# Kernel tuning notes

Measured on AMD Instinct MI355X. Metric: run time of the kernel, lower is better.

## Reference

```python
import jax, jax.numpy as jnp
import numpy as np

B_, L, DM = 4, 1024, 1024
DI, DS, DR, DC = 1024, 16, 64, 4
NH = 4
DK = DM // NH


def setup_inputs() -> dict:
    key = jax.random.key(0)
    ks = jax.random.split(key, 16)
    def w(i, shape, scale=0.02):
        return jax.random.normal(ks[i], shape, dtype=jnp.float32) * scale
    inp = {
        "x": jax.random.normal(ks[0], (B_, L, DM), dtype=jnp.float32),
        "xx": jax.random.normal(ks[1], (B_, L, DI), dtype=jnp.float32),
        "in_proj_w": w(2, (DI, DM)),
        "conv_w": w(3, (DI, 1, DC)),            # depthwise conv, groups=DI
        "conv_b": jnp.zeros((DI,), jnp.float32),
        "x_proj_w": w(4, (DR + 2 * DS, DI)),
        "dt_proj_w": w(5, (DI, DR)),
        "dt_proj_b": jnp.zeros((DI,), jnp.float32),
        "A_log": jnp.log(jnp.tile(jnp.arange(1, DS + 1, dtype=jnp.float32)[None, :], (DI, 1))),
        "D": jnp.ones((DI,), jnp.float32),
        "wq": w(6, (DM, DM)), "bq": jnp.zeros((DM,), jnp.float32),
        "wk": w(7, (DM, DM)), "bk": jnp.zeros((DM,), jnp.float32),
        "wv": w(8, (DM, DM)), "bv": jnp.zeros((DM,), jnp.float32),
        "wo": w(9, (DM, DM)), "bo": jnp.zeros((DM,), jnp.float32),
    }
    return inp


def _stim_forward(x, xx, in_proj_w, conv_w, conv_b, x_proj_w, dt_proj_w, dt_proj_b,
                  A_log, D, wq, bq, wk, bk, wv, bv, wo, bo):
    b, l, _ = xx.shape
    # query branch: in_proj (Linear, no bias)
    q = x @ in_proj_w.T                                    # (b, l, DI)
    # kv branch: causal depthwise conv1d (padding d_conv-1, truncated to l)
    xc = jnp.transpose(xx, (0, 2, 1))                      # (b, DI, l)
    xc = jax.lax.conv_general_dilated(
        xc, conv_w, window_strides=(1,), padding=[(DC - 1, 0)],
        dimension_numbers=("NCH", "OIH", "NCH"), feature_group_count=DI)
    xc = xc + conv_b[None, :, None]
    u = jax.nn.silu(jnp.transpose(xc, (0, 2, 1)))          # (b, l, DI)
    # SSM parameter projections
    A = -jnp.exp(A_log)                                    # (DI, DS)
    x_dbl = u @ x_proj_w.T                                 # (b, l, DR+2*DS)
    delta, Bm, Cm = jnp.split(x_dbl, [DR, DR + DS], axis=-1)
    delta = jax.nn.softplus(delta @ dt_proj_w.T + dt_proj_b)  # (b, l, DI)
    deltaA = jnp.exp(jnp.einsum("bld,dn->bldn", delta, A))    # (b, l, DI, DS)
    deltaBu = jnp.einsum("bld,bln,bld->bldn", delta, Bm, u)   # (b, l, DI, DS)
    # selective scan over time
    def step(h, inp):
        dA_t, dBu_t, C_t = inp
        h = dA_t * h + dBu_t                               # (b, DI, DS)
        y_t = jnp.einsum("bdn,bn->bd", h, C_t)             # (b, DI)
        return h, y_t
    h0 = jnp.zeros((b, DI, DS), dtype=u.dtype)
    _, ys = jax.lax.scan(step, h0, (jnp.moveaxis(deltaA, 1, 0),
                                    jnp.moveaxis(deltaBu, 1, 0),
                                    jnp.moveaxis(Cm, 1, 0)))
    y = jnp.moveaxis(ys, 0, 1) + u * D                     # (b, l, DI)
    # cross attention: query = q, key/value = y
    Q = (q @ wq.T + bq).reshape(b, l, NH, DK).transpose(0, 2, 1, 3)
    K = (y @ wk.T + bk).reshape(b, l, NH, DK).transpose(0, 2, 1, 3)
    V = (y @ wv.T + bv).reshape(b, l, NH, DK).transpose(0, 2, 1, 3)
    scale = 1.0 / np.sqrt(DK).astype(np.float32)
    scores = jnp.einsum("bhqd,bhkd->bhqk", Q, K) * scale
    attn = jax.nn.softmax(scores, axis=-1)
    out = jnp.einsum("bhqk,bhkd->bhqd", attn, V)
    out = out.transpose(0, 2, 1, 3).reshape(b, l, DM)
    return out @ wo.T + bo


def reference(x, xx, in_proj_w, conv_w, conv_b, x_proj_w, dt_proj_w, dt_proj_b,
              A_log, D, wq, bq, wk, bk, wv, bv, wo, bo):
    return _stim_forward(x, xx, in_proj_w, conv_w, conv_b, x_proj_w, dt_proj_w,
                         dt_proj_b, A_log, D, wq, bq, wk, bk, wv, bv, wo, bo)
```

## Files before the change

### kernel.cpp

```cpp
#include <hip/hip_runtime.h>
#include <math.h>

#define B_  4
#define L_  1024
#define DM  1024
#define DI  1024
#define DS  16
#define DR  64
#define DCV 4
#define NH  4
#define DK  256

#define NCH 32
#define CHL (L_ / NCH)

typedef __attribute__((ext_vector_type(8))) short short8;
typedef __attribute__((ext_vector_type(4))) float floatx4;

static __device__ __forceinline__ unsigned short f2bf(float f) {
    unsigned int u = __float_as_uint(f);
    u += 0x7fffu + ((u >> 16) & 1u);
    return (unsigned short)(u >> 16);
}
static __device__ __forceinline__ float bf2f(unsigned short s) {
    return __uint_as_float(((unsigned int)s) << 16);
}

#define GLL(gp, lp) __builtin_amdgcn_global_load_lds( \
        (const __attribute__((address_space(1))) void*)(gp), \
        (__attribute__((address_space(3))) void*)(lp), 16, 0, 0)

static __device__ __forceinline__ void xcd_rect(int gx, int gy, int& tx, int& ty)
{
    int n = blockIdx.x + gx * blockIdx.y;
    if ((gx & 1) == 0 && (gy & 3) == 0) {
        int xcd = n & 7, j = n >> 3;
        int hx = gx >> 1, qy = gy >> 2;
        tx = (xcd & 1) * hx + (j % hx);
        ty = (xcd >> 1) * qy + (j / hx);
    } else {
        tx = blockIdx.x; ty = blockIdx.y;
    }
}

struct PrepArgs {
    const float* xx; const float* cw; const float* cb;
    float* u; unsigned short* ub;
    const float* xs; unsigned short* xd;
    const float* s[6]; unsigned short* d[6];
    int n[6];
    int ns[6];
    const float* tsrc; unsigned short* tdst;
};

__global__ __launch_bounds__(256) void prep(PrepArgs pa)
{
    __shared__ unsigned short tl[32][36];
    int bid = blockIdx.x, tid = threadIdx.x;
    if (bid < 16384) {
        int idx = bid * 256 + tid;
        int d = idx & (DI - 1);
        int l = (idx >> 10) & (L_ - 1);
        int b = idx >> 20;
        const float* xb = pa.xx + (size_t)b * L_ * DI + d;
        float z = pa.cb[d];
#pragma unroll
        for (int j = 0; j < DCV; j++) {
            int t = l - (DCV - 1) + j;
            if (t >= 0) z += xb[(size_t)t * DI] * pa.cw[d * DCV + j];
        }
        float v = z / (1.0f + __expf(-z));
        pa.u[idx] = v;
        pa.ub[idx] = f2bf(v);
        return;
    }
    bid -= 16384;
    if (bid < 4096) {
        int i = (bid * 256 + tid) * 4;
        float4 v = *(const float4*)(pa.xs + i);
        ushort4 o;
        o.x = f2bf(v.x); o.y = f2bf(v.y); o.z = f2bf(v.z); o.w = f2bf(v.w);
        *(ushort4*)(pa.xd + i) = o;
        return;
    }
    bid -= 4096;
#pragma unroll
    for (int r = 0; r < 6; r++) {
        int nb = pa.n[r] >> 10;
        if (bid < nb) {
            int i = (bid * 256 + tid) * 4;
            int ns = pa.ns[r];
            const float* s = pa.s[r];
            ushort4 o;
            if (i + 4 <= ns) {
                float4 v = *(const float4*)(s + i);
                o.x = f2bf(v.x); o.y = f2bf(v.y); o.z = f2bf(v.z); o.w = f2bf(v.w);
            } else {
                float v[4];
#pragma unroll
                for (int j = 0; j < 4; j++) v[j] = (i + j < ns) ? s[i + j] : 0.f;
                o.x = f2bf(v[0]); o.y = f2bf(v[1]); o.z = f2bf(v[2]); o.w = f2bf(v[3]);
            }
            *(ushort4*)(pa.d[r] + i) = o;
            return;
        }
        bid -= nb;
    }
    int j0 = (bid >> 5) * 32;
    int n0 = (bid & 31) * 32;
    int r = tid >> 3, c4 = (tid & 7) * 4;
    float4 v = *(const float4*)(pa.tsrc + (size_t)(j0 + r) * 1024 + n0 + c4);
    tl[r][c4 + 0] = f2bf(v.x); tl[r][c4 + 1] = f2bf(v.y);
    tl[r][c4 + 2] = f2bf(v.z); tl[r][c4 + 3] = f2bf(v.w);
    __syncthreads();
    ushort4 o;
    o.x = tl[c4 + 0][r]; o.y = tl[c4 + 1][r];
    o.z = tl[c4 + 2][r]; o.w = tl[c4 + 3][r];
    *(ushort4*)(pa.tdst + (size_t)(n0 + r) * 1024 + j0 + c4) = o;
}

struct GDesc {
    const unsigned short* A;
    const unsigned short* W;
    const float* bias;
    float* Cf;
    unsigned short* Cb;
    int K, lda, ldw, ldc, ldc2;
    int mode;
    float scale;
    int gx, gy;
};
struct GArgs { GDesc g[3]; };

__global__ __launch_bounds__(256) void gemm_multi(GArgs ga)
{
    GDesc g = ga.g[blockIdx.z];
    int bx, by;
    xcd_rect(gridDim.x, gridDim.y, bx, by);
    if (bx >= g.gx || by >= g.gy) return;

    __shared__ __align__(16) unsigned short Asm[3][128 * 32];
    __shared__ __align__(16) unsigned short Bsm[3][128 * 32];

    int tid = threadIdx.x;
    int wid = tid >> 6;
    int lane = tid & 63;
    int wm = wid & 1, wn = wid >> 1;
    int lr = lane & 15, quad = lane >> 4;
    int sq = quad ^ ((lr >> 1) & 3);

    const unsigned short* Ab = g.A + (size_t)by * 128 * g.lda;
    const unsigned short* Wb = g.W + (size_t)bx * 128 * g.ldw;

    int srow = tid >> 2;
    int scol = ((tid & 3) ^ ((tid >> 3) & 3)) * 8;
    const unsigned short* Ap = Ab + (size_t)srow * g.lda + scol;
    const unsigned short* Wp = Wb + (size_t)srow * g.ldw + scol;

    int lbase = (wid * 16) * 32;

    floatx4 acc[4][4];
#pragma unroll
    for (int i = 0; i < 4; i++)
#pragma unroll
        for (int j = 0; j < 4; j++) acc[i][j] = (floatx4){0.f, 0.f, 0.f, 0.f};

#define STAGE_M(buf) do { \
        GLL(Ap, &Asm[buf][lbase]); \
        GLL(Ap + (size_t)64 * g.lda, &Asm[buf][lbase + 64 * 32]); \
        GLL(Wp, &Bsm[buf][lbase]); \
        GLL(Wp + (size_t)64 * g.ldw, &Bsm[buf][lbase + 64 * 32]); \
        Ap += 32; Wp += 32; \
    } while (0)

    int nK = g.K >> 5;
    STAGE_M(0);
    if (nK > 1) STAGE_M(1);

    int cur = 0, stg = 2;
    for (int k = 0; k < nK - 1; k++) {
        asm volatile("s_waitcnt vmcnt(4)" ::: "memory");
        __builtin_amdgcn_s_barrier();
        __builtin_amdgcn_sched_barrier(0);

        short8 af[4], bf[4];
#pragma unroll
        for (int mt = 0; mt < 4; mt++)
            af[mt] = *(const short8*)&Asm[cur][(wm * 64 + mt * 16 + lr) * 32 + sq * 8];
#pragma unroll
        for (int nt = 0; nt < 4; nt++)
            bf[nt] = *(const short8*)&Bsm[cur][(wn * 64 + nt * 16 + lr) * 32 + sq * 8];

        if (k + 2 < nK) {
            STAGE_M(stg);
            stg = (stg == 2) ? 0 : stg + 1;
        }

        __builtin_amdgcn_s_setprio(1);
#pragma unroll
        for (int mt = 0; mt < 4; mt++)
#pragma unroll
            for (int nt = 0; nt < 4; nt++)
                acc[mt][nt] = __builtin_amdgcn_mfma_f32_16x16x32_bf16(
                    af[mt], bf[nt], acc[mt][nt], 0, 0, 0);
        __builtin_amdgcn_s_setprio(0);
        cur = (cur == 2) ? 0 : cur + 1;
    }
    {
        asm volatile("s_waitcnt vmcnt(0)" ::: "memory");
        __builtin_amdgcn_s_barrier();
        __builtin_amdgcn_sched_barrier(0);

        short8 af[4], bf[4];
#pragma unroll
        for (int mt = 0; mt < 4; mt++)
            af[mt] = *(const short8*)&Asm[cur][(wm * 64 + mt * 16 + lr) * 32 + sq * 8];
#pragma unroll
        for (int nt = 0; nt < 4; nt++)
            bf[nt] = *(const short8*)&Bsm[cur][(wn * 64 + nt * 16 + lr) * 32 + sq * 8];
        __builtin_amdgcn_s_setprio(1);
#pragma unroll
        for (int mt = 0; mt < 4; mt++)
#pragma unroll
            for (int nt = 0; nt < 4; nt++)
                acc[mt][nt] = __builtin_amdgcn_mfma_f32_16x16x32_bf16(
                    af[mt], bf[nt], acc[mt][nt], 0, 0, 0);
        __builtin_amdgcn_s_setprio(0);
    }
#undef STAGE_M

    int bm = by * 128, bn = bx * 128;
    int m = g.mode & 3;
#pragma unroll
    for (int mt = 0; mt < 4; mt++) {
#pragma unroll
        for (int nt = 0; nt < 4; nt++) {
            int row0 = bm + wm * 64 + mt * 16 + quad * 4;
            int col = bn + wn * 64 + nt * 16 + lr;
            float bv = g.bias ? g.bias[col] : 0.f;
#pragma unroll
            for (int i = 0; i < 4; i++) {
                float v = acc[mt][nt][i] * g.scale + bv;
                if (g.mode & 4) v = (v > 15.f) ? v : log1pf(__expf(v));
                if (m == 0) {
                    g.Cf[(size_t)(row0 + i) * g.ldc + col] = v;
                } else if (m == 1) {
                    g.Cb[(size_t)(row0 + i) * g.ldc + col] = f2bf(v);
                } else {
                    g.Cf[(size_t)(row0 + i) * g.ldc + col] = v;
                    g.Cb[(size_t)(row0 + i) * g.ldc2 + col] = f2bf(v);
                }
            }
        }
    }
}

__global__ __launch_bounds__(256) void gemm_batched(
    const unsigned short* __restrict__ A, const unsigned short* __restrict__ W,
    unsigned short* __restrict__ C,
    int K, int lda, int ldw, int ldc,
    long long sA1, long long sA2, long long sW1, long long sW2,
    long long sC1, long long sC2, float scale)
{
    __shared__ __align__(16) unsigned short Asm[3][128 * 32];
    __shared__ __align__(16) unsigned short Bsm[3][128 * 32];

    int bx, by;
    xcd_rect(gridDim.x, gridDim.y, bx, by);

    int z = blockIdx.z;
    long long bq = z >> 2, hq = z & 3;
    int tid = threadIdx.x;
    int wid = tid >> 6;
    int lane = tid & 63;
    int wm = wid & 1, wn = wid >> 1;
    int lr = lane & 15, quad = lane >> 4;
    int sq = quad ^ ((lr >> 1) & 3);

    const unsigned short* Ab = A + bq * sA1 + hq * sA2 + (size_t)by * 128 * lda;
    const unsigned short* Wb = W + bq * sW1 + hq * sW2 + (size_t)bx * 128 * ldw;

    int srow = tid >> 2;
    int scol = ((tid & 3) ^ ((tid >> 3) & 3)) * 8;
    const unsigned short* Ap = Ab + (size_t)srow * lda + scol;
    const unsigned short* Wp = Wb + (size_t)srow * ldw + scol;

    int lbase = (wid * 16) * 32;

    floatx4 acc[4][4];
#pragma unroll
    for (int i = 0; i < 4; i++)
#pragma unroll
        for (int j = 0; j < 4; j++) acc[i][j] = (floatx4){0.f, 0.f, 0.f, 0.f};

#define STAGE_B(buf) do { \
        GLL(Ap, &Asm[buf][lbase]); \
        GLL(Ap + (size_t)64 * lda, &Asm[buf][lbase + 64 * 32]); \
        GLL(Wp, &Bsm[buf][lbase]); \
        GLL(Wp + (size_t)64 * ldw, &Bsm[buf][lbase + 64 * 32]); \
        Ap += 32; Wp += 32; \
    } while (0)

    int nK = K >> 5;
    STAGE_B(0);
    if (nK > 1) STAGE_B(1);

    int cur = 0, stg = 2;
    for (int k = 0; k < nK - 1; k++) {
        asm volatile("s_waitcnt vmcnt(4)" ::: "memory");
        __builtin_amdgcn_s_barrier();
        __builtin_amdgcn_sched_barrier(0);

        short8 af[4], bf[4];
#pragma unroll
        for (int mt = 0; mt < 4; mt++)
            af[mt] = *(const short8*)&Asm[cur][(wm * 64 + mt * 16 + lr) * 32 + sq * 8];
#pragma unroll
        for (int nt = 0; nt < 4; nt++)
            bf[nt] = *(const short8*)&Bsm[cur][(wn * 64 + nt * 16 + lr) * 32 + sq * 8];

        if (k + 2 < nK) {
            STAGE_B(stg);
            stg = (stg == 2) ? 0 : stg + 1;
        }

        __builtin_amdgcn_s_setprio(1);
#pragma unroll
        for (int mt = 0; mt < 4; mt++)
#pragma unroll
            for (int nt = 0; nt < 4; nt++)
                acc[mt][nt] = __builtin_amdgcn_mfma_f32_16x16x32_bf16(
                    af[mt], bf[nt], acc[mt][nt], 0, 0, 0);
        __builtin_amdgcn_s_setprio(0);
        cur = (cur == 2) ? 0 : cur + 1;
    }
    {
        asm volatile("s_waitcnt vmcnt(0)" ::: "memory");
        __builtin_amdgcn_s_barrier();
        __builtin_amdgcn_sched_barrier(0);

        short8 af[4], bf[4];
#pragma unroll
        for (int mt = 0; mt < 4; mt++)
            af[mt] = *(const short8*)&Asm[cur][(wm * 64 + mt * 16 + lr) * 32 + sq * 8];
#pragma unroll
        for (int nt = 0; nt < 4; nt++)
            bf[nt] = *(const short8*)&Bsm[cur][(wn * 64 + nt * 16 + lr) * 32 + sq * 8];
        __builtin_amdgcn_s_setprio(1);
#pragma unroll
        for (int mt = 0; mt < 4; mt++)
#pragma unroll
            for (int nt = 0; nt < 4; nt++)
                acc[mt][nt] = __builtin_amdgcn_mfma_f32_16x16x32_bf16(
                    af[mt], bf[nt], acc[mt][nt], 0, 0, 0);
        __builtin_amdgcn_s_setprio(0);
    }
#undef STAGE_B

    long long coff = bq * sC1 + hq * sC2;
    int bm = by * 128, bn = bx * 128;
    unsigned short* Cb = C + coff;

#pragma unroll
    for (int mt = 0; mt < 4; mt++) {
#pragma unroll
        for (int nt = 0; nt < 4; nt++) {
            int row0 = bm + wm * 64 + mt * 16 + quad * 4;
            int col = bn + wn * 64 + nt * 16 + lr;
#pragma unroll
            for (int i = 0; i < 4; i++)
                Cb[(size_t)(row0 + i) * ldc + col] = f2bf(acc[mt][nt][i] * scale);
        }
    }
}

__global__ __launch_bounds__(256) void scan_a(
    const float* __restrict__ delta, const float* __restrict__ u,
    const float* __restrict__ xdbl, const float* __restrict__ A_log,
    float* __restrict__ Hc, float* __restrict__ sumdv)
{
    int gid = blockIdx.x * 256 + threadIdx.x;
    int c = gid >> 12;
    int bd = gid & 4095;
    int b = bd >> 10, d = bd & 1023;

    float a[16];
#pragma unroll
    for (int j = 0; j < 4; j++) {
        float4 al = *(const float4*)(A_log + d * 16 + j * 4);
        a[j * 4 + 0] = -__expf(al.x); a[j * 4 + 1] = -__expf(al.y);
        a[j * 4 + 2] = -__expf(al.z); a[j * 4 + 3] = -__expf(al.w);
    }
    float h[16];
#pragma unroll
    for (int n = 0; n < 16; n++) h[n] = 0.f;
    float sd = 0.f;

    int t0 = c * CHL;
    const float* dp = delta + ((size_t)(b * L_) + t0) * DI + d;
    const float* up = u + ((size_t)(b * L_) + t0) * DI + d;
    const float* xp = xdbl + ((size_t)(b * L_) + t0) * 128;

#pragma unroll 4
    for (int t = 0; t < CHL; t++) {
        float dv = dp[t * DI];
        float uv = up[t * DI];
        float duv = dv * uv;
        sd += dv;
        float Bv[16];
#pragma unroll
        for (int j = 0; j < 4; j++) {
            float4 bq = *(const float4*)(xp + t * 128 + 64 + j * 4);
            Bv[j * 4 + 0] = bq.x; Bv[j * 4 + 1] = bq.y;
            Bv[j * 4 + 2] = bq.z; Bv[j * 4 + 3] = bq.w;
        }
#pragma unroll
        for (int n = 0; n < 16; n++)
            h[n] = __expf(dv * a[n]) * h[n] + duv * Bv[n];
    }

    float* hp = Hc + ((size_t)c * 4096 + bd) * 16;
#pragma unroll
    for (int j = 0; j < 4; j++)
        *(float4*)(hp + j * 4) = make_float4(h[j * 4], h[j * 4 + 1], h[j * 4 + 2], h[j * 4 + 3]);
    sumdv[c * 4096 + bd] = sd;
}

__global__ __launch_bounds__(256) void scan_b(
    float* __restrict__ Hc, const float* __restrict__ sumdv,
    const float* __restrict__ A_log)
{
    int bd = blockIdx.x * 256 + threadIdx.x;
    int d = bd & 1023;

    float a[16];
#pragma unroll
    for (int j = 0; j < 4; j++) {
        float4 al = *(const float4*)(A_log + d * 16 + j * 4);
        a[j * 4 + 0] = -__expf(al.x); a[j * 4 + 1] = -__expf(al.y);
        a[j * 4 + 2] = -__expf(al.z); a[j * 4 + 3] = -__expf(al.w);
    }
    float H[16];
#pragma unroll
    for (int n = 0; n < 16; n++) H[n] = 0.f;

    for (int c = 0; c < NCH; c++) {
        float* hp = Hc + ((size_t)c * 4096 + bd) * 16;
        float sdv = sumdv[c * 4096 + bd];
        float hc[16];
#pragma unroll
        for (int j = 0; j < 4; j++) {
            float4 q = *(const float4*)(hp + j * 4);
            hc[j * 4 + 0] = q.x; hc[j * 4 + 1] = q.y; hc[j * 4 + 2] = q.z; hc[j * 4 + 3] = q.w;
        }
#pragma unroll
        for (int j = 0; j < 4; j++)
            *(float4*)(hp + j * 4) = make_float4(H[j * 4], H[j * 4 + 1], H[j * 4 + 2], H[j * 4 + 3]);
#pragma unroll
        for (int n = 0; n < 16; n++)
            H[n] = __expf(a[n] * sdv) * H[n] + hc[n];
    }
}

__global__ __launch_bounds__(256) void scan_c(
    const float* __restrict__ delta, const float* __restrict__ u,
    const float* __restrict__ xdbl, const float* __restrict__ A_log,
    const float* __restrict__ Dv, const float* __restrict__ Hstart,
    unsigned short* __restrict__ y)
{
    int gid = blockIdx.x * 256 + threadIdx.x;
    int c = gid >> 12;
    int bd = gid & 4095;
    int b = bd >> 10, d = bd & 1023;

    float a[16];
#pragma unroll
    for (int j = 0; j < 4; j++) {
        float4 al = *(const float4*)(A_log + d * 16 + j * 4);
        a[j * 4 + 0] = -__expf(al.x); a[j * 4 + 1] = -__expf(al.y);
        a[j * 4 + 2] = -__expf(al.z); a[j * 4 + 3] = -__expf(al.w);
    }
    float h[16];
    const float* hp = Hstart + ((size_t)c * 4096 + bd) * 16;
#pragma unroll
    for (int j = 0; j < 4; j++) {
        float4 q = *(const float4*)(hp + j * 4);
        h[j * 4 + 0] = q.x; h[j * 4 + 1] = q.y; h[j * 4 + 2] = q.z; h[j * 4 + 3] = q.w;
    }
    float Dd = Dv[d];

    int t0 = c * CHL;
    const float* dp = delta + ((size_t)(b * L_) + t0) * DI + d;
    const float* up = u + ((size_t)(b * L_) + t0) * DI + d;
    const float* xp = xdbl + ((size_t)(b * L_) + t0) * 128;
    unsigned short* yp = y + ((size_t)(b * L_) + t0) * DI + d;

#pragma unroll 4
    for (int t = 0; t < CHL; t++) {
        float dv = dp[t * DI];
        float uv = up[t * DI];
        float duv = dv * uv;
        float Bv[16], Cv[16];
#pragma unroll
        for (int j = 0; j < 4; j++) {
            float4 bq = *(const float4*)(xp + t * 128 + 64 + j * 4);
            Bv[j * 4 + 0] = bq.x; Bv[j * 4 + 1] = bq.y;
            Bv[j * 4 + 2] = bq.z; Bv[j * 4 + 3] = bq.w;
            float4 cq = *(const float4*)(xp + t * 128 + 80 + j * 4);
            Cv[j * 4 + 0] = cq.x; Cv[j * 4 + 1] = cq.y;
            Cv[j * 4 + 2] = cq.z; Cv[j * 4 + 3] = cq.w;
        }
        float ys = 0.f;
#pragma unroll
        for (int n = 0; n < 16; n++) {
            h[n] = __expf(dv * a[n]) * h[n] + duv * Bv[n];
            ys += h[n] * Cv[n];
        }
        yp[t * DI] = f2bf(ys + uv * Dd);
    }
}

__global__ __launch_bounds__(256) void softmax_transpose(
    unsigned short* __restrict__ S,
    const unsigned short* __restrict__ V, unsigned short* __restrict__ VT)
{
    __shared__ unsigned short tl[32][36];
    int bid = blockIdx.x;
    if (bid < 4096) {
        int row = bid * 4 + (threadIdx.x >> 6);
        int lane = threadIdx.x & 63;
        unsigned short* p = S + (size_t)row * 1024;

        float v[16];
#pragma unroll
        for (int ch = 0; ch < 4; ch++) {
            ushort4 u4 = *(const ushort4*)(p + ch * 256 + lane * 4);
            v[ch * 4 + 0] = bf2f(u4.x); v[ch * 4 + 1] = bf2f(u4.y);
            v[ch * 4 + 2] = bf2f(u4.z); v[ch * 4 + 3] = bf2f(u4.w);
        }
        float m = -1e30f;
#pragma unroll
        for (int i = 0; i < 16; i++) m = fmaxf(m, v[i]);
#pragma unroll
        for (int off = 32; off >= 1; off >>= 1) m = fmaxf(m, __shfl_xor(m, off));
        float s = 0.f;
#pragma unroll
        for (int i = 0; i < 16; i++) { v[i] = __expf(v[i] - m); s += v[i]; }
#pragma unroll
        for (int off = 32; off >= 1; off >>= 1) s += __shfl_xor(s, off);
        float inv = 1.0f / s;
#pragma unroll
        for (int ch = 0; ch < 4; ch++) {
            ushort4 o;
            o.x = f2bf(v[ch * 4 + 0] * inv); o.y = f2bf(v[ch * 4 + 1] * inv);
            o.z = f2bf(v[ch * 4 + 2] * inv); o.w = f2bf(v[ch * 4 + 3] * inv);
            *(ushort4*)(p + ch * 256 + lane * 4) = o;
        }
        return;
    }
    int tb = bid - 4096;
    int bh = tb >> 8;
    int rem = tb & 255;
    int d0 = (rem >> 5) * 32;
    int l0 = (rem & 31) * 32;
    int b = bh >> 2, h = bh & 3;
    int tid = threadIdx.x;
    int r = tid >> 3, c4 = (tid & 7) * 4;

    const unsigned short* src = V + ((size_t)(b * L_ + l0 + r)) * 1024 + h * DK + d0 + c4;
    ushort4 v = *(const ushort4*)src;
    tl[r][c4 + 0] = v.x; tl[r][c4 + 1] = v.y; tl[r][c4 + 2] = v.z; tl[r][c4 + 3] = v.w;
    __syncthreads();

    unsigned short* dst = VT + ((size_t)bh * DK + d0 + r) * L_ + l0 + c4;
    ushort4 o;
    o.x = tl[c4 + 0][r]; o.y = tl[c4 + 1][r]; o.z = tl[c4 + 2][r]; o.w = tl[c4 + 3][r];
    *(ushort4*)dst = o;
}

extern "C" void kernel_launch(void* const* d_in, const int* in_sizes, int n_in,
                              void* d_out, int out_size, void* d_ws, size_t ws_size,
                              hipStream_t stream)
{
    const float* x         = (const float*)d_in[0];
    const float* xx        = (const float*)d_in[1];
    const float* in_proj_w = (const float*)d_in[2];
    const float* conv_w    = (const float*)d_in[3];
    const float* conv_b    = (const float*)d_in[4];
    const float* x_proj_w  = (const float*)d_in[5];
    const float* dt_proj_w = (const float*)d_in[6];
    const float* dt_proj_b = (const float*)d_in[7];
    const float* A_log     = (const float*)d_in[8];
    const float* Dvec      = (const float*)d_in[9];
    const float* wq        = (const float*)d_in[10];
    const float* bq        = (const float*)d_in[11];
    const float* wk        = (const float*)d_in[12];
    const float* bk        = (const float*)d_in[13];
    const float* wv        = (const float*)d_in[14];
    const float* bv        = (const float*)d_in[15];
    const float* wo        = (const float*)d_in[16];
    const float* bo        = (const float*)d_in[17];
    float* out = (float*)d_out;

    char* w = (char*)d_ws;
    const size_t MB = 1024 * 1024, KB = 1024;
    float*          u_f    = (float*)(w + 0);
    float*          delta  = (float*)(w + 16 * MB);
    unsigned short* Sbuf   = (unsigned short*)(w + 0);
    unsigned short* x_bf   = (unsigned short*)(w + 32 * MB);
    unsigned short* Q_bf   = (unsigned short*)(w + 40 * MB);
    unsigned short* VT     = Q_bf;
    unsigned short* y_bf   = (unsigned short*)(w + 48 * MB);
    unsigned short* AO     = y_bf;
    unsigned short* K_bf   = (unsigned short*)(w + 56 * MB);
    unsigned short* V_bf   = (unsigned short*)(w + 64 * MB);
    unsigned short* u_bf   = (unsigned short*)(w + 72 * MB);
    float*          Hc     = (float*)(w + 72 * MB);
    float*          xdbl   = (float*)(w + 80 * MB);
    unsigned short* xdblb  = (unsigned short*)(w + 82 * MB);
    unsigned short* w_inT  = (unsigned short*)(w + 83 * MB);
    unsigned short* w_q    = (unsigned short*)(w + 85 * MB);
    unsigned short* w_k    = (unsigned short*)(w + 87 * MB);
    unsigned short* w_v    = (unsigned short*)(w + 89 * MB);
    unsigned short* w_o    = (unsigned short*)(w + 91 * MB);
    unsigned short* w_xp   = (unsigned short*)(w + 93 * MB);
    unsigned short* w_dt   = (unsigned short*)(w + 93 * MB + 256 * KB);
    float*          sumdv  = (float*)(w + 93 * MB + 384 * KB);
    unsigned short* W_qin  = (unsigned short*)(w + 95 * MB);

    dim3 blk(256);
    const long long LL = L_;

    PrepArgs pa;
    pa.xx = xx; pa.cw = conv_w; pa.cb = conv_b; pa.u = u_f; pa.ub = u_bf;
    pa.xs = x; pa.xd = x_bf;
    pa.s[0] = wq;        pa.d[0] = w_q;  pa.n[0] = 1048576; pa.ns[0] = 1048576;
    pa.s[1] = wk;        pa.d[1] = w_k;  pa.n[1] = 1048576; pa.ns[1] = 1048576;
    pa.s[2] = wv;        pa.d[2] = w_v;  pa.n[2] = 1048576; pa.ns[2] = 1048576;
    pa.s[3] = wo;        pa.d[3] = w_o;  pa.n[3] = 1048576; pa.ns[3] = 1048576;
    pa.s[4] = x_proj_w;  pa.d[4] = w_xp; pa.n[4] = 131072;  pa.ns[4] = 98304;
    pa.s[5] = dt_proj_w; pa.d[5] = w_dt; pa.n[5] = 65536;   pa.ns[5] = 65536;
    pa.tsrc = in_proj_w; pa.tdst = w_inT;
    prep<<<dim3(25792), blk, 0, stream>>>(pa);

    {
        GArgs ga = {};
        ga.g[0] = (GDesc){w_q, w_inT, nullptr, nullptr, W_qin,
                          1024, 1024, 1024, 1024, 0, 1, 1.0f, 8, 8};
        ga.g[1] = (GDesc){u_bf, w_xp, nullptr, xdbl, xdblb,
                          1024, 1024, 1024, 128, 128, 2, 1.0f, 1, 32};
        gemm_multi<<<dim3(8, 32, 2), blk, 0, stream>>>(ga);
    }
    {
        GArgs ga = {};
        ga.g[0] = (GDesc){xdblb, w_dt, dt_proj_b, delta, nullptr,
                          64, 128, 64, 1024, 0, 0 | 4, 1.0f, 8, 32};
        gemm_multi<<<dim3(8, 32, 1), blk, 0, stream>>>(ga);
    }
    scan_a<<<dim3(512), blk, 0, stream>>>(delta, u_f, xdbl, A_log, Hc, sumdv);
    scan_b<<<dim3(16), blk, 0, stream>>>(Hc, sumdv, A_log);
    scan_c<<<dim3(512), blk, 0, stream>>>(delta, u_f, xdbl, A_log, Dvec, Hc, y_bf);

    {
        GArgs ga = {};
        ga.g[0] = (GDesc){x_bf, W_qin, bq, nullptr, Q_bf, 1024, 1024, 1024, 1024, 0, 1, 1.0f, 8, 32};
        ga.g[1] = (GDesc){y_bf, w_k, bk, nullptr, K_bf, 1024, 1024, 1024, 1024, 0, 1, 1.0f, 8, 32};
        ga.g[2] = (GDesc){y_bf, w_v, bv, nullptr, V_bf, 1024, 1024, 1024, 1024, 0, 1, 1.0f, 8, 32};
        gemm_multi<<<dim3(8, 32, 3), blk, 0, stream>>>(ga);
    }
    gemm_batched<<<dim3(8, 8, 16), blk, 0, stream>>>(Q_bf, K_bf, Sbuf,
        DK, 1024, 1024, 1024,
        LL * 1024, 256, LL * 1024, 256,
        4 * LL * 1024, LL * 1024, 0.0625f);
    softmax_transpose<<<dim3(8192), blk, 0, stream>>>(Sbuf, V_bf, VT);
    gemm_batched<<<dim3(2, 8, 16), blk, 0, stream>>>(Sbuf, VT, AO,
        1024, 1024, 1024, 1024,
        4 * LL * 1024, LL * 1024,
        4 * (long long)DK * 1024, (long long)DK * 1024,
        LL * 1024, 256, 1.0f);
    {
        GArgs ga = {};
        ga.g[0] = (GDesc){AO, w_o, bo, out, nullptr, 1024, 1024, 1024, 1024, 0, 0, 1.0f, 8, 32};
        gemm_multi<<<dim3(8, 32, 1), blk, 0, stream>>>(ga);
    }
}
```

Before: 394.8 us.

## Drop fp32 u buffer in scans and split-K the output projection

The conv/SiLU prep no longer writes an fp32 copy of u, and both scan kernels read the bf16 u instead, which cuts global write and read traffic. The final output GEMM is split along K into two halves run as two grid slices, doubling the block count from 256 to 512 so the GPU is better filled. A new elementwise kernel then sums the partials and adds the bias. This costs an extra fp32 partial buffer, another kernel launch, and lower precision for u inside the scan.

```diff
diff --git a/kernel.cpp b/kernel.cpp
--- a/kernel.cpp
+++ b/kernel.cpp
@@ -45,7 +45,7 @@
 
 struct PrepArgs {
     const float* xx; const float* cw; const float* cb;
-    float* u; unsigned short* ub;
+    unsigned short* ub;
     const float* xs; unsigned short* xd;
     const float* s[6]; unsigned short* d[6];
     int n[6];
@@ -70,7 +70,6 @@
             if (t >= 0) z += xb[(size_t)t * DI] * pa.cw[d * DCV + j];
         }
         float v = z / (1.0f + __expf(-z));
-        pa.u[idx] = v;
         pa.ub[idx] = f2bf(v);
         return;
     }
@@ -119,6 +118,20 @@
     *(ushort4*)(pa.tdst + (size_t)(n0 + r) * 1024 + j0 + c4) = o;
 }
 
+__global__ __launch_bounds__(256) void addout(
+    float* __restrict__ out, const float* __restrict__ p1,
+    const float* __restrict__ bias)
+{
+    int i = (blockIdx.x * 256 + threadIdx.x) * 4;
+    int col = i & 1023;
+    float4 a = *(const float4*)(out + i);
+    float4 b = *(const float4*)(p1 + i);
+    float4 bb = *(const float4*)(bias + col);
+    a.x += b.x + bb.x; a.y += b.y + bb.y;
+    a.z += b.z + bb.z; a.w += b.w + bb.w;
+    *(float4*)(out + i) = a;
+}
+
 struct GDesc {
     const unsigned short* A;
     const unsigned short* W;
@@ -375,7 +388,7 @@
 }
 
 __global__ __launch_bounds__(256) void scan_a(
-    const float* __restrict__ delta, const float* __restrict__ u,
+    const float* __restrict__ delta, const unsigned short* __restrict__ u,
     const float* __restrict__ xdbl, const float* __restrict__ A_log,
     float* __restrict__ Hc, float* __restrict__ sumdv)
 {
@@ -398,13 +411,13 @@
 
     int t0 = c * CHL;
     const float* dp = delta + ((size_t)(b * L_) + t0) * DI + d;
-    const float* up = u + ((size_t)(b * L_) + t0) * DI + d;
+    const unsigned short* up = u + ((size_t)(b * L_) + t0) * DI + d;
     const float* xp = xdbl + ((size_t)(b * L_) + t0) * 128;
 
 #pragma unroll 4
     for (int t = 0; t < CHL; t++) {
         float dv = dp[t * DI];
-        float uv = up[t * DI];
+        float uv = bf2f(up[t * DI]);
         float duv = dv * uv;
         sd += dv;
         float Bv[16];
@@ -463,7 +476,7 @@
 }
 
 __global__ __launch_bounds__(256) void scan_c(
-    const float* __restrict__ delta, const float* __restrict__ u,
+    const float* __restrict__ delta, const unsigned short* __restrict__ u,
     const float* __restrict__ xdbl, const float* __restrict__ A_log,
     const float* __restrict__ Dv, const float* __restrict__ Hstart,
     unsigned short* __restrict__ y)
@@ -491,14 +504,14 @@
 
     int t0 = c * CHL;
     const float* dp = delta + ((size_t)(b * L_) + t0) * DI + d;
-    const float* up = u + ((size_t)(b * L_) + t0) * DI + d;
+    const unsigned short* up = u + ((size_t)(b * L_) + t0) * DI + d;
     const float* xp = xdbl + ((size_t)(b * L_) + t0) * 128;
     unsigned short* yp = y + ((size_t)(b * L_) + t0) * DI + d;
 
 #pragma unroll 4
     for (int t = 0; t < CHL; t++) {
         float dv = dp[t * DI];
-        float uv = up[t * DI];
+        float uv = bf2f(up[t * DI]);
         float duv = dv * uv;
         float Bv[16], Cv[16];
 #pragma unroll
@@ -604,7 +617,7 @@
 
     char* w = (char*)d_ws;
     const size_t MB = 1024 * 1024, KB = 1024;
-    float*          u_f    = (float*)(w + 0);
+    float*          Hc     = (float*)(w + 0);
     float*          delta  = (float*)(w + 16 * MB);
     unsigned short* Sbuf   = (unsigned short*)(w + 0);
     unsigned short* x_bf   = (unsigned short*)(w + 32 * MB);
@@ -615,7 +628,6 @@
     unsigned short* K_bf   = (unsigned short*)(w + 56 * MB);
     unsigned short* V_bf   = (unsigned short*)(w + 64 * MB);
     unsigned short* u_bf   = (unsigned short*)(w + 72 * MB);
-    float*          Hc     = (float*)(w + 72 * MB);
     float*          xdbl   = (float*)(w + 80 * MB);
     unsigned short* xdblb  = (unsigned short*)(w + 82 * MB);
     unsigned short* w_inT  = (unsigned short*)(w + 83 * MB);
@@ -627,12 +639,13 @@
     unsigned short* w_dt   = (unsigned short*)(w + 93 * MB + 256 * KB);
     float*          sumdv  = (float*)(w + 93 * MB + 384 * KB);
     unsigned short* W_qin  = (unsigned short*)(w + 95 * MB);
+    float*          p1     = (float*)(w + 97 * MB);
 
     dim3 blk(256);
     const long long LL = L_;
 
     PrepArgs pa;
-    pa.xx = xx; pa.cw = conv_w; pa.cb = conv_b; pa.u = u_f; pa.ub = u_bf;
+    pa.xx = xx; pa.cw = conv_w; pa.cb = conv_b; pa.ub = u_bf;
     pa.xs = x; pa.xd = x_bf;
     pa.s[0] = wq;        pa.d[0] = w_q;  pa.n[0] = 1048576; pa.ns[0] = 1048576;
     pa.s[1] = wk;        pa.d[1] = w_k;  pa.n[1] = 1048576; pa.ns[1] = 1048576;
@@ -657,9 +670,9 @@
                           64, 128, 64, 1024, 0, 0 | 4, 1.0f, 8, 32};
         gemm_multi<<<dim3(8, 32, 1), blk, 0, stream>>>(ga);
     }
-    scan_a<<<dim3(512), blk, 0, stream>>>(delta, u_f, xdbl, A_log, Hc, sumdv);
+    scan_a<<<dim3(512), blk, 0, stream>>>(delta, u_bf, xdbl, A_log, Hc, sumdv);
     scan_b<<<dim3(16), blk, 0, stream>>>(Hc, sumdv, A_log);
-    scan_c<<<dim3(512), blk, 0, stream>>>(delta, u_f, xdbl, A_log, Dvec, Hc, y_bf);
+    scan_c<<<dim3(512), blk, 0, stream>>>(delta, u_bf, xdbl, A_log, Dvec, Hc, y_bf);
 
     {
         GArgs ga = {};
@@ -680,7 +693,11 @@
         LL * 1024, 256, 1.0f);
     {
         GArgs ga = {};
-        ga.g[0] = (GDesc){AO, w_o, bo, out, nullptr, 1024, 1024, 1024, 1024, 0, 0, 1.0f, 8, 32};
-        gemm_multi<<<dim3(8, 32, 1), blk, 0, stream>>>(ga);
-    }
-}
+        ga.g[0] = (GDesc){AO, w_o, nullptr, out, nullptr,
+                          512, 1024, 1024, 1024, 0, 0, 1.0f, 8, 32};
+        ga.g[1] = (GDesc){AO + 512, w_o + 512, nullptr, p1, nullptr,
+                          512, 1024, 1024, 1024, 0, 0, 1.0f, 8, 32};
+        gemm_multi<<<dim3(8, 32, 2), blk, 0, stream>>>(ga);
+    }
+    addout<<<dim3(4096), blk, 0, stream>>>(out, p1, bo);
+}
```

Result: no change. 399.0 us (+1.1%).
